# Kernel tuning notes

Measured on AMD Instinct MI355X. Metric: run time of the kernel, lower is better.

The kernel has to match this reference:

```python
import jax, jax.numpy as jnp
import numpy as np

EPS = 1e-6
DROP_RATE = 0.25

def setup_inputs() -> dict:
    key = jax.random.key(0)
    k1, k2, k3 = jax.random.split(key, 3)
    B, S, D = 4, 2048, 2048
    inputs = jax.random.normal(k1, (B, S, D), dtype=jnp.float32)
    # keras 'uniform' initializer: U(-0.05, 0.05)
    W_1 = jax.random.uniform(k2, (D, D), dtype=jnp.float32, minval=-0.05, maxval=0.05)
    W_2 = jax.random.uniform(k3, (D, D), dtype=jnp.float32, minval=-0.05, maxval=0.05)
    return {"inputs": inputs, "W_1": W_1, "W_2": W_2}

def reference(inputs, W_1, W_2):
    # LayerNorm over last axis (no affine: gamma/beta unused in original call)
    mean = jnp.mean(inputs, axis=-1, keepdims=True)
    var = jnp.mean(jnp.square(inputs - mean), axis=-1, keepdims=True)
    x_norm = (inputs - mean) / jnp.sqrt(var + EPS)          # [B,S,D]
    # 2-layer MLP with relu
    h = jax.nn.relu(jnp.einsum('bsd,de->bse', x_norm, W_1))  # [B,S,D]
    y = jnp.einsum('bsd,de->bse', h, W_2)                    # [B,S,D]
    # dropout(0.25), inverted scaling, fixed key for determinism
    keep = jax.random.bernoulli(jax.random.key(1), 1.0 - DROP_RATE, y.shape)
    y_drop = jnp.where(keep, y / (1.0 - DROP_RATE), 0.0)
    return x_norm + y_drop
```

## Files before the change

### kernel.cpp

```cpp
#include <hip/hip_runtime.h>
#include <hip/hip_bf16.h>
#include <stdint.h>

#define M_DIM 8192
#define N_DIM 2048
#define K_DIM 2048

typedef __bf16 bf16x8_t __attribute__((ext_vector_type(8)));
typedef float f32x4_t __attribute__((ext_vector_type(4)));

__device__ __forceinline__ unsigned tf_rotl(unsigned x, int r) {
  return (x << r) | (x >> (32 - r));
}
__device__ __forceinline__ unsigned threefry_mask_bits(unsigned ctr) {
  unsigned x0 = 0u, x1 = ctr;
  const unsigned ks0 = 0u, ks1 = 1u, ks2 = 0x1BD11BDBu;
  x0 += ks0; x1 += ks1;
#define TFR(r) { x0 += x1; x1 = tf_rotl(x1, (r)); x1 ^= x0; }
  TFR(13) TFR(15) TFR(26) TFR(6)
  x0 += ks1; x1 += ks2 + 1u;
  TFR(17) TFR(29) TFR(16) TFR(24)
  x0 += ks2; x1 += ks0 + 2u;
  TFR(13) TFR(15) TFR(26) TFR(6)
  x0 += ks0; x1 += ks1 + 3u;
  TFR(17) TFR(29) TFR(16) TFR(24)
  x0 += ks1; x1 += ks2 + 4u;
  TFR(13) TFR(15) TFR(26) TFR(6)
  x0 += ks2; x1 += ks0 + 5u;
#undef TFR
  return x0 ^ x1;
}

__device__ __forceinline__ void gload_lds16(const __hip_bfloat16* g, unsigned short* l) {
  __builtin_amdgcn_global_load_lds(
      (const __attribute__((address_space(1))) unsigned int*)g,
      (__attribute__((address_space(3))) unsigned int*)l,
      16, 0, 0);
}

__global__ __launch_bounds__(256) void wt_kernel(
    const float* __restrict__ W1, const float* __restrict__ W2,
    __hip_bfloat16* __restrict__ W1t, __hip_bfloat16* __restrict__ W2t) {
  __shared__ float tile[32][33];
  const float* src = blockIdx.z ? W2 : W1;
  __hip_bfloat16* dst = blockIdx.z ? W2t : W1t;
  int x = blockIdx.x * 32 + threadIdx.x;
  int y = blockIdx.y * 32 + threadIdx.y;
#pragma unroll
  for (int i = 0; i < 32; i += 8)
    tile[threadIdx.y + i][threadIdx.x] = src[(size_t)(y + i) * N_DIM + x];
  __syncthreads();
  int xo = blockIdx.y * 32 + threadIdx.x;
  int yo = blockIdx.x * 32 + threadIdx.y;
#pragma unroll
  for (int i = 0; i < 32; i += 8)
    dst[(size_t)(yo + i) * K_DIM + xo] = __float2bfloat16(tile[threadIdx.x][threadIdx.y + i]);
}

__global__ __launch_bounds__(256) void ln_kernel(const float* __restrict__ X,
                                                 __hip_bfloat16* __restrict__ Xn) {
  const int row = blockIdx.x;
  const float4* xv = (const float4*)(X + (size_t)row * K_DIM);
  float4 v0 = xv[threadIdx.x];
  float4 v1 = xv[threadIdx.x + 256];
  float s  = v0.x + v0.y + v0.z + v0.w + v1.x + v1.y + v1.z + v1.w;
  float ss = v0.x*v0.x + v0.y*v0.y + v0.z*v0.z + v0.w*v0.w
           + v1.x*v1.x + v1.y*v1.y + v1.z*v1.z + v1.w*v1.w;
#pragma unroll
  for (int off = 32; off > 0; off >>= 1) {
    s  += __shfl_xor(s, off);
    ss += __shfl_xor(ss, off);
  }
  __shared__ float rs[4], rss[4];
  const int wave = threadIdx.x >> 6;
  if ((threadIdx.x & 63) == 0) { rs[wave] = s; rss[wave] = ss; }
  __syncthreads();
  float S  = rs[0] + rs[1] + rs[2] + rs[3];
  float SS = rss[0] + rss[1] + rss[2] + rss[3];
  float mean = S * (1.0f / 2048.0f);
  float var  = SS * (1.0f / 2048.0f) - mean * mean;
  float rstd = 1.0f / sqrtf(var + 1e-6f);
  float vv[8] = {v0.x, v0.y, v0.z, v0.w, v1.x, v1.y, v1.z, v1.w};
  unsigned short o[8];
#pragma unroll
  for (int i = 0; i < 8; i++) {
    __hip_bfloat16 b = __float2bfloat16((vv[i] - mean) * rstd);
    o[i] = *(unsigned short*)&b;
  }
  ushort4* dst = (ushort4*)(Xn + (size_t)row * K_DIM);
  dst[threadIdx.x]       = make_ushort4(o[0], o[1], o[2], o[3]);
  dst[threadIdx.x + 256] = make_ushort4(o[4], o[5], o[6], o[7]);
}

template <int EPI>
__global__ __launch_bounds__(512, 2) void gemm256(
    const __hip_bfloat16* __restrict__ A,
    const __hip_bfloat16* __restrict__ Bt,
    const __hip_bfloat16* __restrict__ Xn,
    __hip_bfloat16* __restrict__ Hout,
    float* __restrict__ Fout) {
  __shared__ unsigned short As[2][16384];
  __shared__ unsigned short Bs[2][16384];
  const int tid  = threadIdx.x;
  const int lane = tid & 63;
  const int wave = tid >> 6;
  const int wm = wave >> 2;
  const int wn = wave & 3;

  const int bid = blockIdx.x;
  const int wg  = (bid & 7) * 32 + (bid >> 3);
  const int mBase = (wg & 31) << 8;
  const int nBase = (wg >> 5) << 8;

  f32x4_t acc[8][4];
#pragma unroll
  for (int i = 0; i < 8; i++)
#pragma unroll
    for (int j = 0; j < 4; j++) acc[i][j] = (f32x4_t){0.f, 0.f, 0.f, 0.f};

  const int rowIn = lane >> 3;
  const int csrc  = ((lane & 7) ^ (rowIn & 7)) << 3;
  const __hip_bfloat16* aSrcB = A  + (size_t)(mBase + 8 * wave + rowIn) * K_DIM + csrc;
  const int bRowW = ((wave >> 2) << 6) + ((wave & 3) << 3);
  const __hip_bfloat16* bSrcB = Bt + (size_t)(nBase + bRowW + rowIn) * K_DIM + csrc;
  const int aDst = wave << 9;
  const int bDst = bRowW << 6;

#define STA(b, h, k)                                                                         \
  gload_lds16(aSrcB + (size_t)((h) * 64) * K_DIM + (k), &As[b][aDst + (h) * 4096]);          \
  gload_lds16(aSrcB + (size_t)((h) * 64 + 128) * K_DIM + (k), &As[b][aDst + (h) * 4096 + 8192]);
#define STB(b, h, k)                                                                         \
  gload_lds16(bSrcB + (size_t)((h) * 32) * K_DIM + (k), &Bs[b][bDst + (h) * 2048]);          \
  gload_lds16(bSrcB + (size_t)((h) * 32 + 128) * K_DIM + (k), &Bs[b][bDst + (h) * 2048 + 8192]);

  const int fr = lane & 15;
  const int fq = lane >> 4;
  const int ck0 = ((fq)     ^ (fr & 7)) << 3;
  const int ck1 = ((4 | fq) ^ (fr & 7)) << 3;
  const int aRd = (wm * 128 + fr) * 64;
  const int bRd = (wn * 64  + fr) * 64;

  bf16x8_t aF[4];
  bf16x8_t bK0[4];
  bf16x8_t bK1[4];

#define RDA4(B, MH, CK)                                                       \
  aF[0] = *(const bf16x8_t*)&As[B][aRd + (MH) * 4096 + 0 * 1024 + (CK)];      \
  aF[1] = *(const bf16x8_t*)&As[B][aRd + (MH) * 4096 + 1 * 1024 + (CK)];      \
  aF[2] = *(const bf16x8_t*)&As[B][aRd + (MH) * 4096 + 2 * 1024 + (CK)];      \
  aF[3] = *(const bf16x8_t*)&As[B][aRd + (MH) * 4096 + 3 * 1024 + (CK)];
#define RDB4(B, DST, CK)                                                      \
  DST[0] = *(const bf16x8_t*)&Bs[B][bRd + 0 * 1024 + (CK)];                   \
  DST[1] = *(const bf16x8_t*)&Bs[B][bRd + 1 * 1024 + (CK)];                   \
  DST[2] = *(const bf16x8_t*)&Bs[B][bRd + 2 * 1024 + (CK)];                   \
  DST[3] = *(const bf16x8_t*)&Bs[B][bRd + 3 * 1024 + (CK)];

#define MFMAP(MH, BARR)                                                            \
  _Pragma("unroll")                                                                \
  for (int mi = 0; mi < 4; mi++) {                                                 \
    _Pragma("unroll")                                                              \
    for (int nf = 0; nf < 4; nf++) {                                               \
      acc[(MH) * 4 + mi][nf] = __builtin_amdgcn_mfma_f32_16x16x32_bf16(            \
          aF[mi], BARR[nf], acc[(MH) * 4 + mi][nf], 0, 0, 0);                      \
    }                                                                              \
  }

#define BAR() __builtin_amdgcn_s_barrier()
#define LGKM0() asm volatile("s_waitcnt lgkmcnt(0)" ::: "memory")
#define VMW(n)  asm volatile("s_waitcnt vmcnt(" #n ")" ::: "memory")

#define TILE(T, BUF, OBUF, S1, S3, VMODE)                                \
  {                                                                      \
       \
    RDA4(BUF, 0, ck0) RDB4(BUF, bK0, ck0)                                \
    if (S1) {                                                            \
      STB(OBUF, 0, ((T) + 1) * 64) STB(OBUF, 1, ((T) + 1) * 64)          \
      STA(OBUF, 1, ((T) + 1) * 64)                                       \
    }                                                                    \
    BAR(); LGKM0();                                                      \
    __builtin_amdgcn_s_setprio(1); MFMAP(0, bK0)                         \
    __builtin_amdgcn_s_setprio(0); BAR();                                \
                                                       \
    RDA4(BUF, 0, ck1) RDB4(BUF, bK1, ck1)                                \
    BAR(); LGKM0();                                                      \
    __builtin_amdgcn_s_setprio(1); MFMAP(0, bK1)                         \
    __builtin_amdgcn_s_setprio(0); BAR();                                \
       \
    RDA4(BUF, 1, ck0)                                                    \
    if (S3) { STA(BUF, 0, ((T) + 2) * 64) }                              \
    BAR(); LGKM0();                                                      \
    __builtin_amdgcn_s_setprio(1); MFMAP(1, bK0)                         \
    __builtin_amdgcn_s_setprio(0); BAR();                                \
                            \
    RDA4(BUF, 1, ck1)                                                    \
    if ((VMODE) == 0) { VMW(2); } else if ((VMODE) == 1) { VMW(0); }     \
    BAR(); LGKM0();                                                      \
    __builtin_amdgcn_s_setprio(1); MFMAP(1, bK1)                         \
    __builtin_amdgcn_s_setprio(0); BAR();                                \
  }

  STA(0, 0, 0) STA(0, 1, 0) STB(0, 0, 0) STB(0, 1, 0)
  STA(1, 0, 64)
  VMW(2);
  BAR();

  for (int t = 0; t < 30; t += 2) {
    TILE(t,     0, 1, 1, 1, 0)
    TILE(t + 1, 1, 0, 1, 1, 0)
  }
  TILE(30, 0, 1, 1, 0, 1)
  TILE(31, 1, 0, 0, 0, 2)

#undef TILE
#undef STA
#undef STB
#undef RDA4
#undef RDB4
#undef MFMAP
#undef BAR
#undef LGKM0
#undef VMW

  const int mW = mBase + wm * 128 + fq * 4;
  const int nW = nBase + wn * 64 + fr;
#pragma unroll
  for (int f = 0; f < 8; f++) {
#pragma unroll
    for (int nf = 0; nf < 4; nf++) {
      const int n  = nW + nf * 16;
      const int m0 = mW + f * 16;
#pragma unroll
      for (int r = 0; r < 4; r++) {
        float v = acc[f][nf][r];
        size_t j = (size_t)(m0 + r) * N_DIM + n;
        if (EPI == 0) {
          Hout[j] = __float2bfloat16(fmaxf(v, 0.0f));
        } else {
          unsigned bits = threefry_mask_bits((unsigned)j);
          float y  = (bits < 0xC0000000u) ? v * (1.0f / 0.75f) : 0.0f;
          Fout[j]  = __bfloat162float(Xn[j]) + y;
        }
      }
    }
  }
}

extern "C" void kernel_launch(void* const* d_in, const int* in_sizes, int n_in,
                              void* d_out, int out_size, void* d_ws, size_t ws_size,
                              hipStream_t stream) {
  (void)in_sizes; (void)n_in; (void)out_size; (void)ws_size;
  const float* X  = (const float*)d_in[0];
  const float* W1 = (const float*)d_in[1];
  const float* W2 = (const float*)d_in[2];
  float* out = (float*)d_out;

  unsigned char* ws = (unsigned char*)d_ws;
  __hip_bfloat16* Xn  = (__hip_bfloat16*)(ws);
  __hip_bfloat16* H   = (__hip_bfloat16*)(ws + ((size_t)32 << 20));
  __hip_bfloat16* W1t = (__hip_bfloat16*)(ws + ((size_t)64 << 20));
  __hip_bfloat16* W2t = (__hip_bfloat16*)(ws + ((size_t)72 << 20));

  wt_kernel<<<dim3(64, 64, 2), dim3(32, 8, 1), 0, stream>>>(W1, W2, W1t, W2t);
  ln_kernel<<<M_DIM, 256, 0, stream>>>(X, Xn);
  gemm256<0><<<dim3(256, 1, 1), dim3(512, 1, 1), 0, stream>>>(Xn, W1t, nullptr, H, nullptr);
  gemm256<1><<<dim3(256, 1, 1), dim3(512, 1, 1), 0, stream>>>(H, W2t, Xn, nullptr, out);
}
```

Measured before the change: 341.8 us.

## Shrink GEMM tile to 128x256 and double grid to 512 workgroups

Changes the GEMM block tile from 256x256 to 128x256, halving A's shared-memory buffer and the per-wave accumulators, and launches 512 workgroups instead of 256. The load/MFMA schedule is restructured into four phases that interleave 2-fragment B reads with the global-to-LDS prefetches. The aim is better occupancy and load balance across the MI355X's 256 CUs, since 256 tiles is only one wave of work per CU. The cost is lower arithmetic intensity per tile, which means more global traffic for B and more barriers per unit of MFMA work.

```diff
diff --git a/kernel.cpp b/kernel.cpp
--- a/kernel.cpp
+++ b/kernel.cpp
@@ -93,13 +93,13 @@
 }
 
 template <int EPI>
-__global__ __launch_bounds__(512, 2) void gemm256(
+__global__ __launch_bounds__(512, 2) void gemm128x256(
     const __hip_bfloat16* __restrict__ A,
     const __hip_bfloat16* __restrict__ Bt,
     const __hip_bfloat16* __restrict__ Xn,
     __hip_bfloat16* __restrict__ Hout,
     float* __restrict__ Fout) {
-  __shared__ unsigned short As[2][16384];
+  __shared__ unsigned short As[2][8192];
   __shared__ unsigned short Bs[2][16384];
   const int tid  = threadIdx.x;
   const int lane = tid & 63;
@@ -108,100 +108,94 @@
   const int wn = wave & 3;
 
   const int bid = blockIdx.x;
-  const int wg  = (bid & 7) * 32 + (bid >> 3);
-  const int mBase = (wg & 31) << 8;
-  const int nBase = (wg >> 5) << 8;
-
-  f32x4_t acc[8][4];
-#pragma unroll
-  for (int i = 0; i < 8; i++)
+  const int wg  = (bid & 7) * 64 + (bid >> 3);
+  const int mBase = (wg & 63) << 7;
+  const int nBase = (wg >> 6) << 8;
+
+  f32x4_t acc[4][4];
+#pragma unroll
+  for (int i = 0; i < 4; i++)
 #pragma unroll
     for (int j = 0; j < 4; j++) acc[i][j] = (f32x4_t){0.f, 0.f, 0.f, 0.f};
 
   const int rowIn = lane >> 3;
   const int csrc  = ((lane & 7) ^ (rowIn & 7)) << 3;
   const __hip_bfloat16* aSrcB = A  + (size_t)(mBase + 8 * wave + rowIn) * K_DIM + csrc;
-  const int bRowW = ((wave >> 2) << 6) + ((wave & 3) << 3);
-  const __hip_bfloat16* bSrcB = Bt + (size_t)(nBase + bRowW + rowIn) * K_DIM + csrc;
-  const int aDst = wave << 9;
-  const int bDst = bRowW << 6;
-
-#define STA(b, h, k)                                                                         \
-  gload_lds16(aSrcB + (size_t)((h) * 64) * K_DIM + (k), &As[b][aDst + (h) * 4096]);          \
-  gload_lds16(aSrcB + (size_t)((h) * 64 + 128) * K_DIM + (k), &As[b][aDst + (h) * 4096 + 8192]);
-#define STB(b, h, k)                                                                         \
-  gload_lds16(bSrcB + (size_t)((h) * 32) * K_DIM + (k), &Bs[b][bDst + (h) * 2048]);          \
-  gload_lds16(bSrcB + (size_t)((h) * 32 + 128) * K_DIM + (k), &Bs[b][bDst + (h) * 2048 + 8192]);
+  const __hip_bfloat16* bSrcB = Bt + (size_t)(nBase + 8 * wave + rowIn) * K_DIM + csrc;
+  const int dstW = wave << 9;
+
+#define STA(b, j, k) \
+  gload_lds16(aSrcB + (size_t)((j) * 64) * K_DIM + (k), &As[b][dstW + (j) * 4096]);
+#define STB(b, j, k) \
+  gload_lds16(bSrcB + (size_t)((j) * 64) * K_DIM + (k), &Bs[b][dstW + (j) * 4096]);
 
   const int fr = lane & 15;
   const int fq = lane >> 4;
   const int ck0 = ((fq)     ^ (fr & 7)) << 3;
   const int ck1 = ((4 | fq) ^ (fr & 7)) << 3;
-  const int aRd = (wm * 128 + fr) * 64;
-  const int bRd = (wn * 64  + fr) * 64;
-
-  bf16x8_t aF[4];
-  bf16x8_t bK0[4];
-  bf16x8_t bK1[4];
-
-#define RDA4(B, MH, CK)                                                       \
-  aF[0] = *(const bf16x8_t*)&As[B][aRd + (MH) * 4096 + 0 * 1024 + (CK)];      \
-  aF[1] = *(const bf16x8_t*)&As[B][aRd + (MH) * 4096 + 1 * 1024 + (CK)];      \
-  aF[2] = *(const bf16x8_t*)&As[B][aRd + (MH) * 4096 + 2 * 1024 + (CK)];      \
-  aF[3] = *(const bf16x8_t*)&As[B][aRd + (MH) * 4096 + 3 * 1024 + (CK)];
-#define RDB4(B, DST, CK)                                                      \
-  DST[0] = *(const bf16x8_t*)&Bs[B][bRd + 0 * 1024 + (CK)];                   \
-  DST[1] = *(const bf16x8_t*)&Bs[B][bRd + 1 * 1024 + (CK)];                   \
-  DST[2] = *(const bf16x8_t*)&Bs[B][bRd + 2 * 1024 + (CK)];                   \
-  DST[3] = *(const bf16x8_t*)&Bs[B][bRd + 3 * 1024 + (CK)];
-
-#define MFMAP(MH, BARR)                                                            \
-  _Pragma("unroll")                                                                \
-  for (int mi = 0; mi < 4; mi++) {                                                 \
-    _Pragma("unroll")                                                              \
-    for (int nf = 0; nf < 4; nf++) {                                               \
-      acc[(MH) * 4 + mi][nf] = __builtin_amdgcn_mfma_f32_16x16x32_bf16(            \
-          aF[mi], BARR[nf], acc[(MH) * 4 + mi][nf], 0, 0, 0);                      \
-    }                                                                              \
+  const int aRd = (wm * 64 + fr) * 64;
+  const int bRd = (wn * 64 + fr) * 64;
+
+  bf16x8_t aK[4];
+  bf16x8_t bb[2];
+
+#define RDA4(B, CK)                                                    \
+  aK[0] = *(const bf16x8_t*)&As[B][aRd + 0 * 1024 + (CK)];             \
+  aK[1] = *(const bf16x8_t*)&As[B][aRd + 1 * 1024 + (CK)];             \
+  aK[2] = *(const bf16x8_t*)&As[B][aRd + 2 * 1024 + (CK)];             \
+  aK[3] = *(const bf16x8_t*)&As[B][aRd + 3 * 1024 + (CK)];
+#define RDB2(B, NLO, CK)                                               \
+  bb[0] = *(const bf16x8_t*)&Bs[B][bRd + ((NLO)) * 1024 + (CK)];       \
+  bb[1] = *(const bf16x8_t*)&Bs[B][bRd + ((NLO) + 1) * 1024 + (CK)];
+
+#define MFMA8(NLO)                                                            \
+  _Pragma("unroll")                                                           \
+  for (int mi = 0; mi < 4; mi++) {                                            \
+    _Pragma("unroll")                                                         \
+    for (int nj = 0; nj < 2; nj++) {                                          \
+      acc[mi][(NLO) + nj] = __builtin_amdgcn_mfma_f32_16x16x32_bf16(          \
+          aK[mi], bb[nj], acc[mi][(NLO) + nj], 0, 0, 0);                      \
+    }                                                                         \
   }
 
 #define BAR() __builtin_amdgcn_s_barrier()
 #define LGKM0() asm volatile("s_waitcnt lgkmcnt(0)" ::: "memory")
 #define VMW(n)  asm volatile("s_waitcnt vmcnt(" #n ")" ::: "memory")
 
-#define TILE(T, BUF, OBUF, S1, S3, VMODE)                                \
+#define TILE(T, BUF, OBUF, SE, SP4, VMODE)                               \
   {                                                                      \
-       \
-    RDA4(BUF, 0, ck0) RDB4(BUF, bK0, ck0)                                \
-    if (S1) {                                                            \
-      STB(OBUF, 0, ((T) + 1) * 64) STB(OBUF, 1, ((T) + 1) * 64)          \
-      STA(OBUF, 1, ((T) + 1) * 64)                                       \
-    }                                                                    \
-    BAR(); LGKM0();                                                      \
-    __builtin_amdgcn_s_setprio(1); MFMAP(0, bK0)                         \
-    __builtin_amdgcn_s_setprio(0); BAR();                                \
-                                                       \
-    RDA4(BUF, 0, ck1) RDB4(BUF, bK1, ck1)                                \
-    BAR(); LGKM0();                                                      \
-    __builtin_amdgcn_s_setprio(1); MFMAP(0, bK1)                         \
-    __builtin_amdgcn_s_setprio(0); BAR();                                \
-       \
-    RDA4(BUF, 1, ck0)                                                    \
-    if (S3) { STA(BUF, 0, ((T) + 2) * 64) }                              \
-    BAR(); LGKM0();                                                      \
-    __builtin_amdgcn_s_setprio(1); MFMAP(1, bK0)                         \
-    __builtin_amdgcn_s_setprio(0); BAR();                                \
-                            \
-    RDA4(BUF, 1, ck1)                                                    \
-    if ((VMODE) == 0) { VMW(2); } else if ((VMODE) == 1) { VMW(0); }     \
-    BAR(); LGKM0();                                                      \
-    __builtin_amdgcn_s_setprio(1); MFMAP(1, bK1)                         \
-    __builtin_amdgcn_s_setprio(0); BAR();                                \
-  }
-
-  STA(0, 0, 0) STA(0, 1, 0) STB(0, 0, 0) STB(0, 1, 0)
+                                      \
+    RDA4(BUF, ck0) RDB2(BUF, 0, ck0)                                     \
+    if (SE) { STA(OBUF, 1, ((T) + 1) * 64) }                             \
+    BAR(); LGKM0();                                                      \
+    __builtin_amdgcn_s_setprio(1); MFMA8(0)                              \
+    __builtin_amdgcn_s_setprio(0); BAR();                                \
+                                   \
+    RDB2(BUF, 2, ck0)                                                    \
+    if (SE) { STB(OBUF, 0, ((T) + 1) * 64) STB(OBUF, 1, ((T) + 1) * 64) }\
+    BAR(); LGKM0();                                                      \
+    __builtin_amdgcn_s_setprio(1); MFMA8(2)                              \
+    __builtin_amdgcn_s_setprio(0); BAR();                                \
+                                   \
+    RDA4(BUF, ck1) RDB2(BUF, 0, ck1)                                     \
+    if (SE) { STB(OBUF, 2, ((T) + 1) * 64) STB(OBUF, 3, ((T) + 1) * 64) }\
+    BAR(); LGKM0();                                                      \
+    __builtin_amdgcn_s_setprio(1); MFMA8(0)                              \
+    __builtin_amdgcn_s_setprio(0); BAR();                                \
+    \
+            \
+    RDB2(BUF, 2, ck1)                                                    \
+    if (SP4) { STA(BUF, 0, ((T) + 2) * 64) }                             \
+    if ((VMODE) == 0) { VMW(1); } else if ((VMODE) == 1) { VMW(0); }     \
+    BAR(); LGKM0();                                                      \
+    __builtin_amdgcn_s_setprio(1); MFMA8(2)                              \
+    __builtin_amdgcn_s_setprio(0); BAR();                                \
+  }
+
+  STA(0, 0, 0) STA(0, 1, 0)
+  STB(0, 0, 0) STB(0, 1, 0) STB(0, 2, 0) STB(0, 3, 0)
   STA(1, 0, 64)
-  VMW(2);
+  VMW(1);
   BAR();
 
   for (int t = 0; t < 30; t += 2) {
@@ -215,23 +209,23 @@
 #undef STA
 #undef STB
 #undef RDA4
-#undef RDB4
-#undef MFMAP
+#undef RDB2
+#undef MFMA8
 #undef BAR
 #undef LGKM0
 #undef VMW
 
-  const int mW = mBase + wm * 128 + fq * 4;
+  const int mW = mBase + wm * 64 + fq * 4;
   const int nW = nBase + wn * 64 + fr;
 #pragma unroll
-  for (int f = 0; f < 8; f++) {
+  for (int mi = 0; mi < 4; mi++) {
 #pragma unroll
     for (int nf = 0; nf < 4; nf++) {
       const int n  = nW + nf * 16;
-      const int m0 = mW + f * 16;
+      const int m0 = mW + mi * 16;
 #pragma unroll
       for (int r = 0; r < 4; r++) {
-        float v = acc[f][nf][r];
+        float v = acc[mi][nf][r];
         size_t j = (size_t)(m0 + r) * N_DIM + n;
         if (EPI == 0) {
           Hout[j] = __float2bfloat16(fmaxf(v, 0.0f));
@@ -262,6 +256,6 @@
 
   wt_kernel<<<dim3(64, 64, 2), dim3(32, 8, 1), 0, stream>>>(W1, W2, W1t, W2t);
   ln_kernel<<<M_DIM, 256, 0, stream>>>(X, Xn);
-  gemm256<0><<<dim3(256, 1, 1), dim3(512, 1, 1), 0, stream>>>(Xn, W1t, nullptr, H, nullptr);
-  gemm256<1><<<dim3(256, 1, 1), dim3(512, 1, 1), 0, stream>>>(H, W2t, Xn, nullptr, out);
-}
+  gemm128x256<0><<<dim3(512, 1, 1), dim3(512, 1, 1), 0, stream>>>(Xn, W1t, nullptr, H, nullptr);
+  gemm128x256<1><<<dim3(512, 1, 1), dim3(512, 1, 1), 0, stream>>>(H, W2t, Xn, nullptr, out);
+}
```

New measurement: 373.1 us. 1.09x slower.
